# Kernel optimization log

Hardware: AMD Instinct MI355X
Metric: run time of the kernel (lower is better)

The kernel has to match this reference:

```python
import jax, jax.numpy as jnp
import numpy as np

D_MODEL = 1024
NUM_HEADS = 16
HEAD_WIDTH = 64
SEQ_LEN = 2048
BATCH = 2
NEG_INF = -1e9


def alibi_slopes(num_heads):
    # 2**(-i * 8/num_heads) for i = 1..num_heads, shape [H, 1, 1]
    step = 8.0 / num_heads
    i = jnp.arange(1, num_heads + 1, dtype=jnp.float32)
    return (2.0 ** (-i * step))[:, None, None]


def relative_positions(t_q, t_v):
    # matrix[i, j] = j - i, shape [t_q, t_v]
    return (jnp.arange(t_v)[None, :] - jnp.arange(t_q)[:, None]).astype(jnp.float32)


def setup_inputs() -> dict:
    key = jax.random.key(0)
    ks = jax.random.split(key, 6)
    queries = jax.random.normal(ks[0], (BATCH, SEQ_LEN, D_MODEL), dtype=jnp.float32)
    keys = jax.random.normal(ks[1], (BATCH, SEQ_LEN, D_MODEL), dtype=jnp.float32)
    values = jax.random.normal(ks[2], (BATCH, SEQ_LEN, D_MODEL), dtype=jnp.float32)
    # causal additive mask, broadcastable [1, 1, S, S]
    causal = jnp.where(
        jnp.arange(SEQ_LEN)[None, :] > jnp.arange(SEQ_LEN)[:, None], NEG_INF, 0.0
    ).astype(jnp.float32)[None, None]
    scale = 1.0 / np.sqrt(D_MODEL)
    Wq = jax.random.normal(ks[3], (D_MODEL, D_MODEL), dtype=jnp.float32) * scale
    Wk = jax.random.normal(ks[4], (D_MODEL, D_MODEL), dtype=jnp.float32) * scale
    Wv = jax.random.normal(ks[5], (D_MODEL, D_MODEL), dtype=jnp.float32) * scale
    return {"queries": queries, "keys": keys, "values": values, "mask": causal,
            "Wq": Wq, "Wk": Wk, "Wv": Wv}


def reference(queries, keys, values, mask, Wq, Wk, Wv):
    N, t_q, d = queries.shape
    _, t_v, _ = keys.shape
    H, hw = NUM_HEADS, HEAD_WIDTH

    def split_heads(x, t):
        # [N, t, d] -> [N, H, t, hw]  (nn.Linear: x @ W.T)
        return x.reshape(N, t, H, hw).transpose(0, 2, 1, 3)

    q = split_heads(queries @ Wq.T, t_q)
    k = split_heads(keys @ Wk.T, t_v)
    v = split_heads(values @ Wv.T, t_v)

    att = jnp.einsum("bhqd,bhkd->bhqk", q, k) / np.sqrt(hw)
    # ALiBi bias: slope_h * (j - i), broadcast over batch
    att = att + (alibi_slopes(H) * relative_positions(t_q, t_v))[None]
    att = att + mask[:, :, :t_q, :t_v]
    att = jax.nn.softmax(att, axis=-1)
    res = jnp.einsum("bhqk,bhkd->bhqd", att, v)  # [N, H, t_q, hw]
    return res.transpose(0, 2, 1, 3).reshape(N, t_v, d)
```

## Files before the change

kernel.cpp:

```cpp
#include <hip/hip_runtime.h>
#include <hip/hip_bf16.h>

#define BATCH 2
#define HEADS 16
#define SEQ 2048
#define HW 64
#define DMODEL 1024

typedef unsigned short u16;
typedef __attribute__((ext_vector_type(8))) short short8;
typedef __attribute__((ext_vector_type(4))) float floatx4;

typedef __attribute__((address_space(3))) void* lds_t;
typedef const __attribute__((address_space(1))) void* gbl_t;

__device__ __forceinline__ u16 f2bf(float f) {
    union { float f; unsigned int u; } v; v.f = f;
    unsigned int r = v.u + 0x7fffu + ((v.u >> 16) & 1u);
    return (u16)(r >> 16);
}

__device__ __forceinline__ unsigned int pk2bf(float a, float b) {
    union { __hip_bfloat162 h; unsigned int u; } c;
    c.h = __float22bfloat162_rn(make_float2(a, b));
    return c.u;
}

__global__ __launch_bounds__(256) void conv_kernel(
    const float* __restrict__ s0, const float* __restrict__ s1, const float* __restrict__ s2,
    const float* __restrict__ s3, const float* __restrict__ s4, const float* __restrict__ s5,
    u16* __restrict__ d0, u16* __restrict__ d1, u16* __restrict__ d2,
    u16* __restrict__ d3, u16* __restrict__ d4, u16* __restrict__ d5)
{
    const int z = blockIdx.y;
    const float* src; u16* dst; int n; float mul = 1.0f;
    if (z == 0)      { src = s0; dst = d0; n = BATCH * SEQ * DMODEL; }
    else if (z == 1) { src = s1; dst = d1; n = BATCH * SEQ * DMODEL; }
    else if (z == 2) { src = s2; dst = d2; n = BATCH * SEQ * DMODEL; }
    else if (z == 3) { src = s3; dst = d3; n = DMODEL * DMODEL; }
    else if (z == 4) { src = s4; dst = d4; n = DMODEL * DMODEL; }
    else             { src = s5; dst = d5; n = DMODEL * DMODEL; mul = 0.125f; }

    const int i0 = (blockIdx.x * 256 + threadIdx.x) * 8;
    const int stride = gridDim.x * 256 * 8;
    for (int i = i0; i < n; i += stride) {
        float4 a = *reinterpret_cast<const float4*>(src + i);
        float4 b = *reinterpret_cast<const float4*>(src + i + 4);
        uint4 o;
        o.x = pk2bf(a.x * mul, a.y * mul);
        o.y = pk2bf(a.z * mul, a.w * mul);
        o.z = pk2bf(b.x * mul, b.y * mul);
        o.w = pk2bf(b.z * mul, b.w * mul);
        *reinterpret_cast<uint4*>(dst + i) = o;
    }
}

__global__ __launch_bounds__(256) void proj_bf16_kernel(
    const u16* __restrict__ Xk, const u16* __restrict__ Xv, const u16* __restrict__ Xq,
    const u16* __restrict__ Wk, const u16* __restrict__ Wv, const u16* __restrict__ Wq,
    u16* __restrict__ Ok, u16* __restrict__ Ov, u16* __restrict__ Oq)
{
    const u16* X; const u16* W;
    if (blockIdx.z == 0)      { X = Xk; W = Wk; }
    else if (blockIdx.z == 1) { X = Xv; W = Wv; }
    else                      { X = Xq; W = Wq; }

    __shared__ u16 As[128][64];
    __shared__ u16 Bs[128][64];

    const int tid = threadIdx.x;
    const int lane = tid & 63, wave = tid >> 6;
    const int quad = lane >> 4, l15 = lane & 15;
    const int swz = l15 & 7;
    const int wm = (wave >> 1) << 6, wn = (wave & 1) << 6;
    const int tm = blockIdx.y, tn = blockIdx.x;

    const int srow = (wave << 5) + (lane >> 3);
    const int scol = (((lane & 7) ^ (lane >> 3)) << 3);
    const u16* gA = X + (size_t)(tm * 128 + srow) * DMODEL + scol;
    const u16* gB = W + (size_t)(tn * 128 + srow) * DMODEL + scol;

    floatx4 acc[4][4];
    for (int i = 0; i < 4; i++) for (int j = 0; j < 4; j++) acc[i][j] = (floatx4)0.0f;

    for (int k0 = 0; k0 < DMODEL; k0 += 64) {
        for (int j = 0; j < 4; j++) {
            __builtin_amdgcn_global_load_lds((gbl_t)(gA + (size_t)j * 8 * DMODEL + k0),
                (lds_t)(&As[(wave << 5) + (j << 3)][0]), 16, 0, 0);
            __builtin_amdgcn_global_load_lds((gbl_t)(gB + (size_t)j * 8 * DMODEL + k0),
                (lds_t)(&Bs[(wave << 5) + (j << 3)][0]), 16, 0, 0);
        }
        __syncthreads();
        {
            short8 af[4], bf[4];
            for (int i = 0; i < 4; i++)
                af[i] = *reinterpret_cast<const short8*>(&As[wm + i * 16 + l15][(quad ^ swz) << 3]);
            for (int j = 0; j < 4; j++)
                bf[j] = *reinterpret_cast<const short8*>(&Bs[wn + j * 16 + l15][(quad ^ swz) << 3]);
            for (int i = 0; i < 4; i++)
                for (int j = 0; j < 4; j++)
                    acc[i][j] = __builtin_amdgcn_mfma_f32_16x16x32_bf16(af[i], bf[j], acc[i][j], 0, 0, 0);
            for (int i = 0; i < 4; i++)
                af[i] = *reinterpret_cast<const short8*>(&As[wm + i * 16 + l15][((quad + 4) ^ swz) << 3]);
            for (int j = 0; j < 4; j++)
                bf[j] = *reinterpret_cast<const short8*>(&Bs[wn + j * 16 + l15][((quad + 4) ^ swz) << 3]);
            for (int i = 0; i < 4; i++)
                for (int j = 0; j < 4; j++)
                    acc[i][j] = __builtin_amdgcn_mfma_f32_16x16x32_bf16(af[i], bf[j], acc[i][j], 0, 0, 0);
        }
        __syncthreads();
    }

    if (blockIdx.z != 1) {
        u16* O = (blockIdx.z == 0) ? Ok : Oq;
        for (int i = 0; i < 4; i++) for (int j = 0; j < 4; j++) {
            int n = (tn << 7) + wn + (j << 4) + l15;
            int h = n >> 6, d = n & 63;
            for (int r = 0; r < 4; r++) {
                int m = (tm << 7) + wm + (i << 4) + (quad << 2) + r;
                int b = m >> 11, s = m & 2047;
                int pc = (((d >> 3) ^ (s & 7)) << 3) | (d & 7);
                O[(size_t)((((b << 4) + h) << 11) + s) * 64 + pc] = f2bf(acc[i][j][r]);
            }
        }
    } else {
        for (int i = 0; i < 4; i++) for (int j = 0; j < 4; j++) {
            int n = (tn << 7) + wn + (j << 4) + l15;
            int h = n >> 6, d = n & 63;
            int m = (tm << 7) + wm + (i << 4) + (quad << 2);
            int b = m >> 11, s0 = m & 2047;
            int ps = (s0 & ~63) | (((((s0 >> 3) & 7) ^ (d & 7)) << 3)) | (s0 & 7);
            uint2 pk;
            pk.x = pk2bf(acc[i][j][0], acc[i][j][1]);
            pk.y = pk2bf(acc[i][j][2], acc[i][j][3]);
            *reinterpret_cast<uint2*>(Ov + ((size_t)(((b << 4) + h) << 6) + d) * SEQ + ps) = pk;
        }
    }
}

__global__ __launch_bounds__(256) void proj_f32_kernel(
    const float* __restrict__ Xk, const float* __restrict__ Xv, const float* __restrict__ Xq,
    const float* __restrict__ Wk, const float* __restrict__ Wv, const float* __restrict__ Wq,
    u16* __restrict__ Ok, u16* __restrict__ Ov, u16* __restrict__ Oq)
{
    const float* X; const float* W;
    if (blockIdx.z == 0)      { X = Xk; W = Wk; }
    else if (blockIdx.z == 1) { X = Xv; W = Wv; }
    else                      { X = Xq; W = Wq; }

    __shared__ u16 As[128][72];
    __shared__ u16 Bs[128][72];

    const int tid = threadIdx.x;
    const int lane = tid & 63, wave = tid >> 6;
    const int quad = lane >> 4, l15 = lane & 15;
    const int wm = (wave >> 1) << 6, wn = (wave & 1) << 6;
    const int tm = blockIdx.y, tn = blockIdx.x;

    const int sr = tid >> 4;
    const int sc = (tid & 15) << 2;
    const float* Xp = X + (size_t)(tm * 128 + sr) * DMODEL + sc;
    const float* Wp = W + (size_t)(tn * 128 + sr) * DMODEL + sc;

    float4 ra[8], rb[8];
#define PLOAD(K0) \
    for (int i = 0; i < 8; i++) { \
        ra[i] = *reinterpret_cast<const float4*>(Xp + (size_t)16 * i * DMODEL + (K0)); \
        rb[i] = *reinterpret_cast<const float4*>(Wp + (size_t)16 * i * DMODEL + (K0)); \
    }

    floatx4 acc[4][4];
    for (int i = 0; i < 4; i++) for (int j = 0; j < 4; j++) acc[i][j] = (floatx4)0.0f;

    PLOAD(0);
    for (int k0 = 0; k0 < DMODEL; k0 += 64) {
        for (int i = 0; i < 8; i++) {
            uint2 pa; pa.x = pk2bf(ra[i].x, ra[i].y); pa.y = pk2bf(ra[i].z, ra[i].w);
            *reinterpret_cast<uint2*>(&As[sr + 16 * i][sc]) = pa;
            uint2 pb; pb.x = pk2bf(rb[i].x, rb[i].y); pb.y = pk2bf(rb[i].z, rb[i].w);
            *reinterpret_cast<uint2*>(&Bs[sr + 16 * i][sc]) = pb;
        }
        __syncthreads();
        if (k0 + 64 < DMODEL) { PLOAD(k0 + 64); }
        for (int kc = 0; kc < 2; kc++) {
            short8 af[4], bf[4];
            for (int i = 0; i < 4; i++)
                af[i] = *reinterpret_cast<const short8*>(&As[wm + i * 16 + l15][kc * 32 + quad * 8]);
            for (int j = 0; j < 4; j++)
                bf[j] = *reinterpret_cast<const short8*>(&Bs[wn + j * 16 + l15][kc * 32 + quad * 8]);
            for (int i = 0; i < 4; i++)
                for (int j = 0; j < 4; j++)
                    acc[i][j] = __builtin_amdgcn_mfma_f32_16x16x32_bf16(af[i], bf[j], acc[i][j], 0, 0, 0);
        }
        __syncthreads();
    }
#undef PLOAD

    if (blockIdx.z != 1) {
        u16* O = (blockIdx.z == 0) ? Ok : Oq;
        const float mul = (blockIdx.z == 0) ? 1.0f : 0.125f;
        for (int i = 0; i < 4; i++) for (int j = 0; j < 4; j++) {
            int n = (tn << 7) + wn + (j << 4) + l15;
            int h = n >> 6, d = n & 63;
            for (int r = 0; r < 4; r++) {
                int m = (tm << 7) + wm + (i << 4) + (quad << 2) + r;
                int b = m >> 11, s = m & 2047;
                int pc = (((d >> 3) ^ (s & 7)) << 3) | (d & 7);
                O[(size_t)((((b << 4) + h) << 11) + s) * 64 + pc] = f2bf(acc[i][j][r] * mul);
            }
        }
    } else {
        for (int i = 0; i < 4; i++) for (int j = 0; j < 4; j++) {
            int n = (tn << 7) + wn + (j << 4) + l15;
            int h = n >> 6, d = n & 63;
            int m = (tm << 7) + wm + (i << 4) + (quad << 2);
            int b = m >> 11, s0 = m & 2047;
            int ps = (s0 & ~63) | (((((s0 >> 3) & 7) ^ (d & 7)) << 3)) | (s0 & 7);
            uint2 pk;
            pk.x = pk2bf(acc[i][j][0], acc[i][j][1]);
            pk.y = pk2bf(acc[i][j][2], acc[i][j][3]);
            *reinterpret_cast<uint2*>(Ov + ((size_t)(((b << 4) + h) << 6) + d) * SEQ + ps) = pk;
        }
    }
}

__global__ __launch_bounds__(256) void attn_kernel(
    const u16* __restrict__ Qg, const u16* __restrict__ K,
    const u16* __restrict__ VtG, float* __restrict__ out)
{
    __shared__ u16 smem[16896];
    u16* Pst = smem + 12288;

    const int tid = threadIdx.x;
    const int lane = tid & 63, wave = tid >> 6;
    const int quad = lane >> 4, l15 = lane & 15;

    const int bid = blockIdx.x;
    const int qt = 31 - (bid >> 5);
    const int bh = bid & 31;
    const int b = bh >> 4, h = bh & 15;
    const float slope = exp2f(-0.5f * (float)(h + 1));
    const int q0 = qt << 6;
    const int swz = l15 & 7;

    const u16* Qh  = Qg  + (size_t)bh * SEQ * HW;
    const u16* Kh  = K   + (size_t)bh * SEQ * HW;
    const u16* Vth = VtG + (size_t)bh * HW * SEQ;

#define ISSUE_K(KV, BUF) do { \
    const u16* gk_ = Kh + (size_t)((KV) + wave * 16) * 64 + lane * 8; \
    __builtin_amdgcn_global_load_lds((gbl_t)gk_, (lds_t)(smem + (BUF) * 4096 + wave * 1024), 16, 0, 0); \
    __builtin_amdgcn_global_load_lds((gbl_t)(gk_ + 512), (lds_t)(smem + (BUF) * 4096 + wave * 1024 + 512), 16, 0, 0); \
} while (0)
#define ISSUE_V(KV) do { \
    const u16* gv_ = Vth + (size_t)(wave * 16 + (lane >> 3)) * SEQ + (KV) + (lane & 7) * 8; \
    __builtin_amdgcn_global_load_lds((gbl_t)gv_, (lds_t)(smem + 8192 + wave * 1024), 16, 0, 0); \
    __builtin_amdgcn_global_load_lds((gbl_t)(gv_ + 8 * SEQ), (lds_t)(smem + 8192 + wave * 1024 + 512), 16, 0, 0); \
} while (0)

    {
        const u16* gq = Qh + (size_t)(q0 + wave * 16) * 64 + lane * 8;
        __builtin_amdgcn_global_load_lds((gbl_t)gq, (lds_t)(smem + 8192 + wave * 1024), 16, 0, 0);
        __builtin_amdgcn_global_load_lds((gbl_t)(gq + 512), (lds_t)(smem + 8192 + wave * 1024 + 512), 16, 0, 0);
    }
    asm volatile("s_waitcnt vmcnt(0)" ::: "memory");
    short8 qf[2];
    qf[0] = *reinterpret_cast<const short8*>(smem + 8192 + (wave * 16 + l15) * 64 + ((quad ^ swz) << 3));
    qf[1] = *reinterpret_cast<const short8*>(smem + 8192 + (wave * 16 + l15) * 64 + (((quad + 4) ^ swz) << 3));
    asm volatile("s_waitcnt lgkmcnt(0)" ::: "memory");
    __builtin_amdgcn_sched_barrier(0);

    ISSUE_K(0, 0);

    const float L2E = 1.44269504088896340736f;
    const float MB  = 12.0f * L2E;
    const int qg = q0 + (wave << 4) + l15;
    const float SL = slope * L2E;

    float lpart = 0.0f;
    floatx4 acc_o[4];
    for (int t = 0; t < 4; t++) acc_o[t] = (floatx4)0.0f;

    for (int kt = 0; kt <= qt; kt++) {
        const int kv0 = kt << 6;
        asm volatile("s_waitcnt vmcnt(0)" ::: "memory");
        __builtin_amdgcn_s_barrier();
        __builtin_amdgcn_sched_barrier(0);
        ISSUE_V(kv0);
        if (kt < qt) { ISSUE_K(kv0 + 64, (kt + 1) & 1); }

        const u16* Kbase = smem + (kt & 1) * 4096;
        floatx4 sv[4];
        __builtin_amdgcn_s_setprio(1);
        for (int t = 0; t < 4; t++) {
            short8 kf0 = *reinterpret_cast<const short8*>(Kbase + (t * 16 + l15) * 64 + ((quad ^ swz) << 3));
            short8 kf1 = *reinterpret_cast<const short8*>(Kbase + (t * 16 + l15) * 64 + (((quad + 4) ^ swz) << 3));
            floatx4 s = (floatx4)0.0f;
            s = __builtin_amdgcn_mfma_f32_16x16x32_bf16(kf0, qf[0], s, 0, 0, 0);
            s = __builtin_amdgcn_mfma_f32_16x16x32_bf16(kf1, qf[1], s, 0, 0, 0);
            sv[t] = s;
        }
        __builtin_amdgcn_s_setprio(0);

        u16* Pt = Pst + wave * 1152;
        if (kt < qt) {
            const float b0 = fmaf(SL, (float)(kv0 + (quad << 2) - qg), -MB);
            for (int t = 0; t < 4; t++) {
                float p0 = __builtin_amdgcn_exp2f(fmaf(sv[t][0], L2E, fmaf(SL, (float)(t * 16 + 0), b0)));
                float p1 = __builtin_amdgcn_exp2f(fmaf(sv[t][1], L2E, fmaf(SL, (float)(t * 16 + 1), b0)));
                float p2 = __builtin_amdgcn_exp2f(fmaf(sv[t][2], L2E, fmaf(SL, (float)(t * 16 + 2), b0)));
                float p3 = __builtin_amdgcn_exp2f(fmaf(sv[t][3], L2E, fmaf(SL, (float)(t * 16 + 3), b0)));
                lpart += (p0 + p1) + (p2 + p3);
                uint2 pk; pk.x = pk2bf(p0, p1); pk.y = pk2bf(p2, p3);
                *reinterpret_cast<uint2*>(Pt + l15 * 72 + t * 16 + (quad << 2)) = pk;
            }
        } else {
            const float fb = (float)(kv0 + (quad << 2) - qg);
            for (int t = 0; t < 4; t++) {
                float p[4];
                for (int r = 0; r < 4; r++) {
                    float rel = fb + (float)(t * 16 + r);
                    float bd = fmaf(fminf(slope * rel, -1e9f * rel), L2E, -MB);
                    p[r] = __builtin_amdgcn_exp2f(fmaf(sv[t][r], L2E, bd));
                }
                lpart += (p[0] + p[1]) + (p[2] + p[3]);
                uint2 pk; pk.x = pk2bf(p[0], p[1]); pk.y = pk2bf(p[2], p[3]);
                *reinterpret_cast<uint2*>(Pt + l15 * 72 + t * 16 + (quad << 2)) = pk;
            }
        }

        if (kt < qt) { asm volatile("s_waitcnt vmcnt(2)" ::: "memory"); }
        else         { asm volatile("s_waitcnt vmcnt(0)" ::: "memory"); }
        __builtin_amdgcn_s_barrier();
        __builtin_amdgcn_sched_barrier(0);

        short8 pf0 = *reinterpret_cast<const short8*>(Pt + l15 * 72 + quad * 8);
        short8 pf1 = *reinterpret_cast<const short8*>(Pt + l15 * 72 + 32 + quad * 8);
        __builtin_amdgcn_s_setprio(1);
        for (int t2 = 0; t2 < 4; t2++) {
            short8 vf0 = *reinterpret_cast<const short8*>(smem + 8192 + (t2 * 16 + l15) * 64 + ((quad ^ swz) << 3));
            short8 vf1 = *reinterpret_cast<const short8*>(smem + 8192 + (t2 * 16 + l15) * 64 + (((quad + 4) ^ swz) << 3));
            acc_o[t2] = __builtin_amdgcn_mfma_f32_16x16x32_bf16(vf0, pf0, acc_o[t2], 0, 0, 0);
            acc_o[t2] = __builtin_amdgcn_mfma_f32_16x16x32_bf16(vf1, pf1, acc_o[t2], 0, 0, 0);
        }
        __builtin_amdgcn_s_setprio(0);
    }
#undef ISSUE_K
#undef ISSUE_V

    float l_run = lpart;
    l_run += __shfl_xor(l_run, 16);
    l_run += __shfl_xor(l_run, 32);
    const float inv = 1.0f / l_run;

    float* op = out + (size_t)(b * SEQ + qg) * DMODEL + h * 64;
    for (int t2 = 0; t2 < 4; t2++) {
        float4 o;
        o.x = acc_o[t2][0] * inv; o.y = acc_o[t2][1] * inv;
        o.z = acc_o[t2][2] * inv; o.w = acc_o[t2][3] * inv;
        *reinterpret_cast<float4*>(op + t2 * 16 + (quad << 2)) = o;
    }
}

extern "C" void kernel_launch(void* const* d_in, const int* in_sizes, int n_in,
                              void* d_out, int out_size, void* d_ws, size_t ws_size,
                              hipStream_t stream) {
    const float* q  = (const float*)d_in[0];
    const float* k  = (const float*)d_in[1];
    const float* v  = (const float*)d_in[2];
    const float* wq = (const float*)d_in[4];
    const float* wk = (const float*)d_in[5];
    const float* wv = (const float*)d_in[6];
    float* out = (float*)d_out;

    const size_t he = (size_t)BATCH * HEADS * SEQ * HW;
    const size_t we = (size_t)DMODEL * DMODEL;
    u16* Kb  = (u16*)d_ws;
    u16* VtB = Kb + he;
    u16* Qb  = VtB + he;

    const size_t need_A = (size_t)(6 * he) * sizeof(u16);
    const bool pathA = (ws_size >= need_A) && ((size_t)out_size >= 3 * we * sizeof(u16));

    if (pathA) {
        u16* Xkb = Qb + he;
        u16* Xvb = Xkb + he;
        u16* Xqb = Xvb + he;
        u16* Wkb = (u16*)d_out;
        u16* Wvb = Wkb + we;
        u16* Wqb = Wvb + we;
        conv_kernel<<<dim3(512, 6), 256, 0, stream>>>(k, v, q, wk, wv, wq,
                                                      Xkb, Xvb, Xqb, Wkb, Wvb, Wqb);
        proj_bf16_kernel<<<dim3(DMODEL / 128, (BATCH * SEQ) / 128, 3), 256, 0, stream>>>(
            Xkb, Xvb, Xqb, Wkb, Wvb, Wqb, Kb, VtB, Qb);
    } else {
        proj_f32_kernel<<<dim3(DMODEL / 128, (BATCH * SEQ) / 128, 3), 256, 0, stream>>>(
            k, v, q, wk, wv, wq, Kb, VtB, Qb);
    }
    attn_kernel<<<BATCH * HEADS * (SEQ / 64), 256, 0, stream>>>(Qb, Kb, VtB, out);
}
```

Baseline: 207.7 us.

## Fuse activation bf16 conversion into projection GEMM with register prefetch

Drops the separate pass that converted the three fp32 activation tensors to bf16 in workspace. The projection kernel now loads fp32 activations into registers, converts and stores them to a padded LDS tile, and prefetches the next k-slice while the MFMAs run. Only the weights are still pre-converted. A flat grid remaps blocks so that row tiles group by XCD. This saves a full read/write round trip of the activations and one launch, at the cost of more registers and VALU conversion work inside the GEMM loop, plus an unswizzled padded A tile.

```diff
diff --git a/kernel.cpp b/kernel.cpp
--- a/kernel.cpp
+++ b/kernel.cpp
@@ -26,46 +26,43 @@
     return c.u;
 }
 
-__global__ __launch_bounds__(256) void conv_kernel(
-    const float* __restrict__ s0, const float* __restrict__ s1, const float* __restrict__ s2,
-    const float* __restrict__ s3, const float* __restrict__ s4, const float* __restrict__ s5,
-    u16* __restrict__ d0, u16* __restrict__ d1, u16* __restrict__ d2,
-    u16* __restrict__ d3, u16* __restrict__ d4, u16* __restrict__ d5)
+__global__ __launch_bounds__(256) void convw_kernel(
+    const float* __restrict__ wk, const float* __restrict__ wv, const float* __restrict__ wq,
+    u16* __restrict__ ok, u16* __restrict__ ov, u16* __restrict__ oq)
 {
     const int z = blockIdx.y;
-    const float* src; u16* dst; int n; float mul = 1.0f;
-    if (z == 0)      { src = s0; dst = d0; n = BATCH * SEQ * DMODEL; }
-    else if (z == 1) { src = s1; dst = d1; n = BATCH * SEQ * DMODEL; }
-    else if (z == 2) { src = s2; dst = d2; n = BATCH * SEQ * DMODEL; }
-    else if (z == 3) { src = s3; dst = d3; n = DMODEL * DMODEL; }
-    else if (z == 4) { src = s4; dst = d4; n = DMODEL * DMODEL; }
-    else             { src = s5; dst = d5; n = DMODEL * DMODEL; mul = 0.125f; }
-
-    const int i0 = (blockIdx.x * 256 + threadIdx.x) * 8;
-    const int stride = gridDim.x * 256 * 8;
-    for (int i = i0; i < n; i += stride) {
-        float4 a = *reinterpret_cast<const float4*>(src + i);
-        float4 b = *reinterpret_cast<const float4*>(src + i + 4);
-        uint4 o;
-        o.x = pk2bf(a.x * mul, a.y * mul);
-        o.y = pk2bf(a.z * mul, a.w * mul);
-        o.z = pk2bf(b.x * mul, b.y * mul);
-        o.w = pk2bf(b.z * mul, b.w * mul);
-        *reinterpret_cast<uint4*>(dst + i) = o;
-    }
-}
-
-__global__ __launch_bounds__(256) void proj_bf16_kernel(
-    const u16* __restrict__ Xk, const u16* __restrict__ Xv, const u16* __restrict__ Xq,
-    const u16* __restrict__ Wk, const u16* __restrict__ Wv, const u16* __restrict__ Wq,
+    const float* src; u16* dst; float mul = 1.0f;
+    if (z == 0)      { src = wk; dst = ok; }
+    else if (z == 1) { src = wv; dst = ov; }
+    else             { src = wq; dst = oq; mul = 0.125f; }
+
+    const int i = (blockIdx.x * 256 + threadIdx.x) * 8;
+    float4 a = *reinterpret_cast<const float4*>(src + i);
+    float4 b = *reinterpret_cast<const float4*>(src + i + 4);
+    uint4 o;
+    o.x = pk2bf(a.x * mul, a.y * mul);
+    o.y = pk2bf(a.z * mul, a.w * mul);
+    o.z = pk2bf(b.x * mul, b.y * mul);
+    o.w = pk2bf(b.z * mul, b.w * mul);
+    *reinterpret_cast<uint4*>(dst + i) = o;
+}
+
+__global__ __launch_bounds__(256) void proj_kernel(
+    const float* __restrict__ Xk, const float* __restrict__ Xv, const float* __restrict__ Xq,
+    const u16* __restrict__ Wb,
     u16* __restrict__ Ok, u16* __restrict__ Ov, u16* __restrict__ Oq)
 {
-    const u16* X; const u16* W;
-    if (blockIdx.z == 0)      { X = Xk; W = Wk; }
-    else if (blockIdx.z == 1) { X = Xv; W = Wv; }
-    else                      { X = Xq; W = Wq; }
-
-    __shared__ u16 As[128][64];
+    const int bid = blockIdx.x;
+    const int xcd = bid & 7, idx = bid >> 3;
+    const int z = idx >> 5;
+    const int r = idx & 31;
+    const int tm = (xcd << 2) | (r >> 3);
+    const int tn = r & 7;
+
+    const float* X = (z == 0) ? Xk : (z == 1) ? Xv : Xq;
+    const u16* W = Wb + (size_t)z * DMODEL * DMODEL;
+
+    __shared__ u16 As[128][72];
     __shared__ u16 Bs[128][64];
 
     const int tid = threadIdx.x;
@@ -73,54 +70,58 @@
     const int quad = lane >> 4, l15 = lane & 15;
     const int swz = l15 & 7;
     const int wm = (wave >> 1) << 6, wn = (wave & 1) << 6;
-    const int tm = blockIdx.y, tn = blockIdx.x;
-
-    const int srow = (wave << 5) + (lane >> 3);
-    const int scol = (((lane & 7) ^ (lane >> 3)) << 3);
-    const u16* gA = X + (size_t)(tm * 128 + srow) * DMODEL + scol;
-    const u16* gB = W + (size_t)(tn * 128 + srow) * DMODEL + scol;
+
+    const int sr = tid >> 4;
+    const int sc = (tid & 15) << 2;
+    const float* Xp = X + (size_t)(tm * 128 + sr) * DMODEL + sc;
+
+    const int srowB = (wave << 5) + (lane >> 3);
+    const int scolB = (((lane & 7) ^ (lane >> 3)) << 3);
+    const u16* gB = W + (size_t)(tn * 128 + srowB) * DMODEL + scolB;
+
+    float4 ra[8];
+#define PLOAD(K0) \
+    for (int i = 0; i < 8; i++) \
+        ra[i] = *reinterpret_cast<const float4*>(Xp + (size_t)16 * i * DMODEL + (K0));
 
     floatx4 acc[4][4];
     for (int i = 0; i < 4; i++) for (int j = 0; j < 4; j++) acc[i][j] = (floatx4)0.0f;
 
+    PLOAD(0);
     for (int k0 = 0; k0 < DMODEL; k0 += 64) {
-        for (int j = 0; j < 4; j++) {
-            __builtin_amdgcn_global_load_lds((gbl_t)(gA + (size_t)j * 8 * DMODEL + k0),
-                (lds_t)(&As[(wave << 5) + (j << 3)][0]), 16, 0, 0);
+        for (int j = 0; j < 4; j++)
             __builtin_amdgcn_global_load_lds((gbl_t)(gB + (size_t)j * 8 * DMODEL + k0),
                 (lds_t)(&Bs[(wave << 5) + (j << 3)][0]), 16, 0, 0);
+        for (int i = 0; i < 8; i++) {
+            uint2 pa; pa.x = pk2bf(ra[i].x, ra[i].y); pa.y = pk2bf(ra[i].z, ra[i].w);
+            *reinterpret_cast<uint2*>(&As[sr + 16 * i][sc]) = pa;
         }
         __syncthreads();
-        {
+        if (k0 + 64 < DMODEL) { PLOAD(k0 + 64); }
+        for (int kc = 0; kc < 2; kc++) {
             short8 af[4], bf[4];
             for (int i = 0; i < 4; i++)
-                af[i] = *reinterpret_cast<const short8*>(&As[wm + i * 16 + l15][(quad ^ swz) << 3]);
+                af[i] = *reinterpret_cast<const short8*>(&As[wm + i * 16 + l15][kc * 32 + quad * 8]);
             for (int j = 0; j < 4; j++)
-                bf[j] = *reinterpret_cast<const short8*>(&Bs[wn + j * 16 + l15][(quad ^ swz) << 3]);
+                bf[j] = *reinterpret_cast<const short8*>(&Bs[wn + j * 16 + l15][((kc * 4 + quad) ^ swz) << 3]);
             for (int i = 0; i < 4; i++)
                 for (int j = 0; j < 4; j++)
                     acc[i][j] = __builtin_amdgcn_mfma_f32_16x16x32_bf16(af[i], bf[j], acc[i][j], 0, 0, 0);
-            for (int i = 0; i < 4; i++)
-                af[i] = *reinterpret_cast<const short8*>(&As[wm + i * 16 + l15][((quad + 4) ^ swz) << 3]);
-            for (int j = 0; j < 4; j++)
-                bf[j] = *reinterpret_cast<const short8*>(&Bs[wn + j * 16 + l15][((quad + 4) ^ swz) << 3]);
-            for (int i = 0; i < 4; i++)
-                for (int j = 0; j < 4; j++)
-                    acc[i][j] = __builtin_amdgcn_mfma_f32_16x16x32_bf16(af[i], bf[j], acc[i][j], 0, 0, 0);
         }
         __syncthreads();
     }
-
-    if (blockIdx.z != 1) {
-        u16* O = (blockIdx.z == 0) ? Ok : Oq;
+#undef PLOAD
+
+    if (z != 1) {
+        u16* O = (z == 0) ? Ok : Oq;
         for (int i = 0; i < 4; i++) for (int j = 0; j < 4; j++) {
             int n = (tn << 7) + wn + (j << 4) + l15;
             int h = n >> 6, d = n & 63;
-            for (int r = 0; r < 4; r++) {
-                int m = (tm << 7) + wm + (i << 4) + (quad << 2) + r;
+            for (int rr = 0; rr < 4; rr++) {
+                int m = (tm << 7) + wm + (i << 4) + (quad << 2) + rr;
                 int b = m >> 11, s = m & 2047;
                 int pc = (((d >> 3) ^ (s & 7)) << 3) | (d & 7);
-                O[(size_t)((((b << 4) + h) << 11) + s) * 64 + pc] = f2bf(acc[i][j][r]);
+                O[(size_t)((((b << 4) + h) << 11) + s) * 64 + pc] = f2bf(acc[i][j][rr]);
             }
         }
     } else {
@@ -379,20 +380,10 @@
     u16* VtB = Kb + he;
     u16* Qb  = VtB + he;
 
-    const size_t need_A = (size_t)(6 * he) * sizeof(u16);
-    const bool pathA = (ws_size >= need_A) && ((size_t)out_size >= 3 * we * sizeof(u16));
-
-    if (pathA) {
-        u16* Xkb = Qb + he;
-        u16* Xvb = Xkb + he;
-        u16* Xqb = Xvb + he;
-        u16* Wkb = (u16*)d_out;
-        u16* Wvb = Wkb + we;
-        u16* Wqb = Wvb + we;
-        conv_kernel<<<dim3(512, 6), 256, 0, stream>>>(k, v, q, wk, wv, wq,
-                                                      Xkb, Xvb, Xqb, Wkb, Wvb, Wqb);
-        proj_bf16_kernel<<<dim3(DMODEL / 128, (BATCH * SEQ) / 128, 3), 256, 0, stream>>>(
-            Xkb, Xvb, Xqb, Wkb, Wvb, Wqb, Kb, VtB, Qb);
+    if ((size_t)out_size >= 3 * we * sizeof(u16)) {
+        u16* Wb = (u16*)d_out;
+        convw_kernel<<<dim3(512, 3), 256, 0, stream>>>(wk, wv, wq, Wb, Wb + we, Wb + 2 * we);
+        proj_kernel<<<768, 256, 0, stream>>>(k, v, q, Wb, Kb, VtB, Qb);
     } else {
         proj_f32_kernel<<<dim3(DMODEL / 128, (BATCH * SEQ) / 128, 3), 256, 0, stream>>>(
             k, v, q, wk, wv, wq, Kb, VtB, Qb);
```

Result: no change. 209.0 us (+0.6%).
